# Kernel optimization log

Measured on AMD Instinct MI355X. Metric: run time of the kernel, lower is better.

## Reference

```python
import jax, jax.numpy as jnp
import numpy as np

N_HEAD = 32


def _apply_rope(x, rope):
    # x: (B, H, T, hs); rope: (block_size, hs//2) angles
    B, H, T, hs = x.shape
    ang = rope[:T]  # (T, hs//2)
    cos = jnp.cos(ang)[None, :, None, :]  # (1, T, 1, hs//2)
    sin = jnp.sin(ang)[None, :, None, :]
    xt = x.transpose(0, 2, 1, 3).reshape(B, T, H, hs // 2, 2)
    x0, x1 = xt[..., 0], xt[..., 1]
    out_r = x0 * cos - x1 * sin
    out_i = x0 * sin + x1 * cos
    out = jnp.stack([out_r, out_i], axis=-1).reshape(B, T, H, hs)
    return out.transpose(0, 2, 1, 3)


def setup_inputs() -> dict:
    key = jax.random.key(0)
    ks = jax.random.split(key, 6)
    B, T, C = 2, 2048, 4096
    aT = 10
    hs = C // N_HEAD
    return {
        "x": jax.random.normal(ks[0], (B, T, C), dtype=jnp.float32),
        "adaption_prompt": jax.random.normal(ks[1], (1, aT, C), dtype=jnp.float32),
        "rope_cache": jax.random.uniform(ks[2], (4096, hs // 2), dtype=jnp.float32) * 2.0 * np.pi,
        "w_attn": jax.random.normal(ks[3], (C, 3 * C), dtype=jnp.float32) * 0.02,
        "w_proj": jax.random.normal(ks[4], (C, C), dtype=jnp.float32) * 0.02,
        "gating_factor": jax.random.normal(ks[5], (1,), dtype=jnp.float32) * 0.1,
    }


def reference(x, adaption_prompt, rope_cache, w_attn, w_proj, gating_factor):
    B, T, C = x.shape
    H = N_HEAD
    hs = C // H

    qkv = x @ w_attn  # (B, T, 3C)
    q, k, v = jnp.split(qkv, 3, axis=2)
    q = q.reshape(B, T, H, hs).transpose(0, 2, 1, 3)  # (B, H, T, hs)
    k = k.reshape(B, T, H, hs).transpose(0, 2, 1, 3)
    v = v.reshape(B, T, H, hs).transpose(0, 2, 1, 3)

    q = _apply_rope(q, rope_cache)
    k = _apply_rope(k, rope_cache)

    # causal SDPA, scale = 1/sqrt(head_size)
    scale = 1.0 / jnp.sqrt(jnp.asarray(hs, dtype=q.dtype))
    scores = jnp.einsum("bhqd,bhkd->bhqk", q, k) * scale
    causal = jnp.tril(jnp.ones((T, T), dtype=bool))
    scores = jnp.where(causal[None, None, :, :], scores, jnp.asarray(-jnp.inf, scores.dtype))
    attn = jax.nn.softmax(scores, axis=-1)
    y = jnp.einsum("bhqk,bhkd->bhqd", attn, v)  # (B, H, T, hs)

    # adapter attention (note: scale uses full n_embd, as in source)
    aT = adaption_prompt.shape[1]
    aqkv = adaption_prompt @ w_attn  # (1, aT, 3C)
    _, ak, av = jnp.split(aqkv, 3, axis=2)
    ak = ak.reshape(1, aT, H, hs).transpose(0, 2, 1, 3)  # (1, H, aT, hs)
    av = av.reshape(1, aT, H, hs).transpose(0, 2, 1, 3)
    ascores = jnp.einsum("bhqd,xhkd->bhqk", q, ak) / jnp.sqrt(jnp.asarray(C, q.dtype))
    ascores = gating_factor[0] * jax.nn.softmax(ascores.astype(jnp.float32), axis=-1).astype(q.dtype)
    y = y + jnp.einsum("bhqk,xhkd->bhqd", ascores, av)

    y = y.transpose(0, 2, 1, 3).reshape(B, T, C)
    return y @ w_proj
```

## Files before the change

### kernel.cpp

```cpp
#include <hip/hip_runtime.h>

typedef unsigned short u16;
typedef unsigned int u32;
typedef __attribute__((ext_vector_type(4))) float f32x4;
typedef __attribute__((ext_vector_type(8))) _Float16 half8;
typedef __attribute__((ext_vector_type(8))) unsigned short u16x8;
typedef __attribute__((ext_vector_type(4))) unsigned short u16x4;

static __device__ __forceinline__ u16 f2h(float f) {
  union { _Float16 h; u16 u; } c;
  c.h = (_Float16)f;
  return c.u;
}
static __device__ __forceinline__ float h2f(u16 u) {
  union { _Float16 h; u16 u; } c;
  c.u = u;
  return (float)c.h;
}
static __device__ __forceinline__ void gload_lds16(const void* g, void* l) {
  __builtin_amdgcn_global_load_lds((const __attribute__((address_space(1))) void*)g,
                                   (__attribute__((address_space(3))) void*)l,
                                   16, 0, 0);
}

__global__ __launch_bounds__(256) void transpose_cvt(const float* __restrict__ src,
                                                     u16* __restrict__ dst,
                                                     int R, int C) {
  __shared__ float tt[64][65];
  const int t = threadIdx.x;
  const int c0 = blockIdx.x << 6, r0 = blockIdx.y << 6;
  const int r = t >> 4, cb = (t & 15) << 2;
#pragma unroll
  for (int i = 0; i < 4; ++i) {
    f32x4 v = *(const f32x4*)(src + (size_t)(r0 + r + i * 16) * C + c0 + cb);
#pragma unroll
    for (int j = 0; j < 4; ++j) tt[cb + j][r + i * 16] = v[j];
  }
  __syncthreads();
  const int cc = t >> 2, r8 = (t & 3) << 4;
  u16x8 o0, o1;
#pragma unroll
  for (int j = 0; j < 8; ++j) o0[j] = f2h(tt[cc][r8 + j]);
#pragma unroll
  for (int j = 0; j < 8; ++j) o1[j] = f2h(tt[cc][r8 + 8 + j]);
  u16* dp = dst + (size_t)(c0 + cc) * R + r0 + r8;
  *(u16x8*)dp = o0;
  *(u16x8*)(dp + 8) = o1;
}

__global__ __launch_bounds__(256) void cvt_f32_f16(const float* __restrict__ in,
                                                   u16* __restrict__ out, int n4) {
  int i = blockIdx.x * 256 + threadIdx.x;
  if (i >= n4) return;
  f32x4 v = *(const f32x4*)(in + (size_t)i * 4);
  u16x4 o;
  o[0] = f2h(v[0]); o[1] = f2h(v[1]); o[2] = f2h(v[2]); o[3] = f2h(v[3]);
  *(u16x4*)(out + (size_t)i * 4) = o;
}

static __device__ __forceinline__ void store_out(float* C, size_t idx, float v) { C[idx] = v; }
static __device__ __forceinline__ void store_out(u16* C, size_t idx, float v) { C[idx] = f2h(v); }

static __device__ __forceinline__ void stageA(const u16* __restrict__ Ab, int K, int kt,
                                              u16* As, int mh, int t) {
  int hf = t >> 8;
  int tt = t & 255;
  int row = hf * 128 + mh * 32 + (tt >> 3);
  int slot = tt & 7;
  gload_lds16(Ab + (size_t)row * K + kt + ((slot ^ (row & 7)) << 3),
              (char*)As + hf * 16384 + mh * 4096 + tt * 16);
}
static __device__ __forceinline__ void stageB(const u16* __restrict__ Bb, int K, int kt,
                                              u16* Bs, int j, int t) {
  int row = j * 64 + (t >> 3);
  int slot = t & 7;
  gload_lds16(Bb + (size_t)row * K + kt + ((slot ^ (row & 7)) << 3),
              (char*)Bs + j * 8192 + t * 16);
}

#define LOAD_BF(BS)                                                              \
  _Pragma("unroll") for (int nf = 0; nf < 4; ++nf)                               \
    _Pragma("unroll") for (int kk = 0; kk < 2; ++kk) {                           \
      int row = wn * 64 + nf * 16 + l15;                                         \
      int slot = (kk * 4 + g) ^ (l15 & 7);                                       \
      bf[nf][kk] = *(const half8*)((const char*)(BS) + row * 128 + slot * 16);   \
    }

#define LOAD_AF(AF, AS, Q)                                                       \
  _Pragma("unroll") for (int mf = 0; mf < 2; ++mf)                               \
    _Pragma("unroll") for (int kk = 0; kk < 2; ++kk) {                           \
      int row = wm * 128 + ((Q) * 2 + mf) * 16 + l15;                            \
      int slot = (kk * 4 + g) ^ (l15 & 7);                                       \
      (AF)[mf][kk] = *(const half8*)((const char*)(AS) + row * 128 + slot * 16); \
    }

#define MFMA_BURST(AF, Q)                                                        \
  __builtin_amdgcn_s_setprio(1);                                                 \
  _Pragma("unroll") for (int kk = 0; kk < 2; ++kk)                               \
    _Pragma("unroll") for (int mf = 0; mf < 2; ++mf)                             \
      _Pragma("unroll") for (int nf = 0; nf < 4; ++nf)                           \
        acc[(Q) * 2 + mf][nf] = __builtin_amdgcn_mfma_f32_16x16x32_f16(          \
            (AF)[mf][kk], bf[nf][kk], acc[(Q) * 2 + mf][nf], 0, 0, 0);           \
  __builtin_amdgcn_s_setprio(0);

template <typename OutT>
__global__ __launch_bounds__(512, 2) void gemm256(const u16* __restrict__ A,
                                                  const u16* __restrict__ Bt,
                                                  OutT* __restrict__ C,
                                                  u16* __restrict__ vtg,
                                                  int M, int N, int K, int nbn,
                                                  int ldc) {
  __shared__ u16 lds[4][16384];
  const int t = threadIdx.x;
  const int lane = t & 63;
  const int wid = t >> 6;
  const int g = lane >> 4, l15 = lane & 15;
  const int wm = wid >> 2, wn = wid & 3;
  const int nwg = gridDim.x;
  const int bid = blockIdx.x;
  const int wgid = (bid & 7) * (nwg >> 3) + (bid >> 3);
  const int bm = wgid / nbn, bn = wgid % nbn;
  const u16* Ab = A + (size_t)bm * 256 * K;
  const u16* Bb = Bt + (size_t)bn * 256 * K;
  f32x4 acc[8][4] = {};

  stageA(Ab, K, 0, lds[0], 0, t);
  stageA(Ab, K, 0, lds[0], 1, t);
  stageA(Ab, K, 0, lds[0], 2, t);
  stageA(Ab, K, 0, lds[0], 3, t);
  stageB(Bb, K, 0, lds[1], 0, t);
  stageB(Bb, K, 0, lds[1], 1, t);
  stageB(Bb, K, 0, lds[1], 2, t);
  stageB(Bb, K, 0, lds[1], 3, t);
  asm volatile("s_waitcnt vmcnt(0)" ::: "memory");
  __builtin_amdgcn_s_barrier();

  const int nt = K >> 6;
  for (int i = 0; i < nt; ++i) {
    u16* As  = lds[(i & 1) << 1];
    u16* Bs  = lds[((i & 1) << 1) + 1];
    u16* Asn = lds[((i + 1) & 1) << 1];
    u16* Bsn = lds[(((i + 1) & 1) << 1) + 1];
    int k1 = (i + 1) << 6; if (k1 >= K) k1 = 0;
    half8 bf[4][2], afA[2][2], afB[2][2];
    LOAD_BF(Bs);
    LOAD_AF(afA, As, 0);
    stageB(Bb, K, k1, Bsn, 0, t);
    stageB(Bb, K, k1, Bsn, 1, t);
    stageB(Bb, K, k1, Bsn, 2, t);
    stageB(Bb, K, k1, Bsn, 3, t);
    stageA(Ab, K, k1, Asn, 0, t);
    stageA(Ab, K, k1, Asn, 1, t);
    stageA(Ab, K, k1, Asn, 2, t);
    stageA(Ab, K, k1, Asn, 3, t);
    LOAD_AF(afB, As, 1);
    MFMA_BURST(afA, 0);
    LOAD_AF(afA, As, 2);
    MFMA_BURST(afB, 1);
    LOAD_AF(afB, As, 3);
    MFMA_BURST(afA, 2);
    MFMA_BURST(afB, 3);
    asm volatile("s_waitcnt vmcnt(0) lgkmcnt(0)" ::: "memory");
    __builtin_amdgcn_s_barrier();
  }

  if (vtg && bn >= 32) {
#pragma unroll
    for (int mf = 0; mf < 8; ++mf) {
      int row0 = bm * 256 + wm * 128 + mf * 16 + 4 * g;
      int bI = row0 >> 11, t0 = row0 & 2047;
#pragma unroll
      for (int nf = 0; nf < 4; ++nf) {
        int vcol = bn * 256 + wn * 64 + nf * 16 + l15 - 8192;
        int hI = vcol >> 7, dI = vcol & 127;
        u16x4 o;
#pragma unroll
        for (int r = 0; r < 4; ++r) o[r] = f2h(acc[mf][nf][r]);
        *(u16x4*)(vtg + ((size_t)(bI * 32 + hI) * 128 + dI) * 2048 + t0) = o;
      }
    }
  } else {
#pragma unroll
    for (int mf = 0; mf < 8; ++mf) {
      int row0 = bm * 256 + wm * 128 + mf * 16 + 4 * g;
#pragma unroll
      for (int nf = 0; nf < 4; ++nf) {
        int col = bn * 256 + wn * 64 + nf * 16 + l15;
#pragma unroll
        for (int r = 0; r < 4; ++r)
          store_out(C, (size_t)(row0 + r) * ldc + col, acc[mf][nf][r]);
      }
    }
  }
}

__global__ __launch_bounds__(256) void rope_kernel(u16* __restrict__ qk,
                                                   const float* __restrict__ rope) {
  int idx = blockIdx.x * 256 + threadIdx.x;
  int bt = idx >> 12;
  int pp = idx & 4095;
  int part = pp >> 11;
  int within = pp & 2047;
  int hh = within >> 6;
  int p = within & 63;
  int tpos = bt & 2047;
  size_t off = (size_t)bt * 8192 + part * 4096 + hh * 128 + 2 * p;
  u32* ptr = (u32*)(qk + off);
  u32 v = *ptr;
  float x0 = h2f((u16)(v & 0xffff));
  float x1 = h2f((u16)(v >> 16));
  float sn, cs;
  __sincosf(rope[tpos * 64 + p], &sn, &cs);
  float y0 = x0 * cs - x1 * sn;
  float y1 = x0 * sn + x1 * cs;
  *ptr = (u32)f2h(y0) | ((u32)f2h(y1) << 16);
}

__global__ __launch_bounds__(256) void adaption_kv_kernel(const float* __restrict__ prompt,
                                                          const float* __restrict__ w_attn,
                                                          u16* __restrict__ akbuf,
                                                          u16* __restrict__ avbuf) {
  __shared__ float pl[10][512];
  __shared__ float red[8][10][32];
  const int t = threadIdx.x;
  const int tc = t & 31, tk = t >> 5;
  const int n = blockIdx.x * 32 + tc;
  float acc[10] = {};
  for (int k0 = 0; k0 < 4096; k0 += 512) {
    __syncthreads();
#pragma unroll
    for (int i = 0; i < 20; ++i) {
      int idx = t + 256 * i;
      int j = idx >> 9, kk = idx & 511;
      pl[j][kk] = prompt[(size_t)j * 4096 + k0 + kk];
    }
    __syncthreads();
    for (int kk = tk; kk < 512; kk += 8) {
      float wv = w_attn[(size_t)(k0 + kk) * 12288 + 4096 + n];
#pragma unroll
      for (int j = 0; j < 10; ++j) acc[j] += pl[j][kk] * wv;
    }
  }
  __syncthreads();
#pragma unroll
  for (int j = 0; j < 10; ++j) red[tk][j][tc] = acc[j];
  __syncthreads();
  if (tk == 0) {
    float s[10];
#pragma unroll
    for (int j = 0; j < 10; ++j) {
      s[j] = 0.f;
#pragma unroll
      for (int q = 0; q < 8; ++q) s[j] += red[q][j][tc];
    }
    u16* dst;
    int hh, d;
    if (n < 4096) { dst = akbuf; hh = n >> 7; d = n & 127; }
    else          { dst = avbuf; hh = (n - 4096) >> 7; d = n & 127; }
#pragma unroll
    for (int j = 0; j < 16; ++j)
      dst[(size_t)(hh * 16 + j) * 128 + d] = (j < 10) ? f2h(s[j]) : (u16)0;
  }
}

__global__ __launch_bounds__(256) void attn_kernel(const u16* __restrict__ qk,
                                                   const u16* __restrict__ vt,
                                                   const u16* __restrict__ akbuf,
                                                   const u16* __restrict__ avbuf,
                                                   const float* __restrict__ gating,
                                                   u16* __restrict__ y) {
  __shared__ u16 Kl[64 * 128];
  __shared__ u16 Vtl[128 * 64];
  __shared__ u16 Pl[4][16 * 64];

  const int t = threadIdx.x;
  const int lane = t & 63, w = t >> 6;
  const int g = lane >> 4, l15 = lane & 15;
  const int bx = blockIdx.x;
  const int qb = 31 - (bx >> 6);
  const int bh = bx & 63, b = bh >> 5, h = bh & 31;
  const int ldq = 8192;
  const u16* Qg = qk + (size_t)b * 2048 * ldq + h * 128;
  const u16* Kg = Qg + 4096;
  const u16* VtG = vt + (size_t)(b * 32 + h) * 128 * 2048;
  u16* AKb = &Pl[0][0];

#pragma unroll
  for (int i = 0; i < 4; ++i) {
    int c = t + 256 * i;
    int row = c >> 4, slot = c & 15;
    gload_lds16(Qg + (size_t)(qb * 64 + row) * ldq + ((slot ^ (row & 15)) << 3),
                (char*)Kl + c * 16);
  }
  {
    int row = t >> 4, slot = t & 15;
    gload_lds16(akbuf + (size_t)(h * 16 + row) * 128 + ((slot ^ row) << 3),
                (char*)AKb + t * 16);
  }
  __syncthreads();

  half8 qf[4];
#pragma unroll
  for (int kk = 0; kk < 4; ++kk) {
    int slot = (kk * 4 + g) ^ l15;
    qf[kk] = *(const half8*)((const char*)Kl + (w * 16 + l15) * 256 + (slot << 4));
  }
  f32x4 sa = {};
#pragma unroll
  for (int kk = 0; kk < 4; ++kk) {
    int slot = (kk * 4 + g) ^ l15;
    half8 af = *(const half8*)((const char*)AKb + l15 * 256 + (slot << 4));
    sa = __builtin_amdgcn_mfma_f32_16x16x32_f16(qf[kk], af, sa, 0, 0, 0);
  }
  __syncthreads();

  f32x4 acc[8] = {};
  float mrun[4], lrun[4];
#pragma unroll
  for (int r = 0; r < 4; ++r) { mrun[r] = -1e30f; lrun[r] = 0.f; }

  for (int kvt = 0; kvt <= qb; ++kvt) {
#pragma unroll
    for (int i = 0; i < 4; ++i) {
      int c = t + 256 * i;
      int row = c >> 4, slot = c & 15;
      gload_lds16(Kg + (size_t)(kvt * 64 + row) * ldq + ((slot ^ (row & 15)) << 3),
                  (char*)Kl + c * 16);
    }
#pragma unroll
    for (int i = 0; i < 4; ++i) {
      int c = t + 256 * i;
      int d = c >> 3, s3 = c & 7;
      gload_lds16(VtG + (size_t)d * 2048 + kvt * 64 + ((s3 ^ (d & 7)) << 3),
                  (char*)Vtl + c * 16);
    }
    __syncthreads();

    f32x4 s[4] = {};
#pragma unroll
    for (int nf = 0; nf < 4; ++nf) {
#pragma unroll
      for (int kk = 0; kk < 4; ++kk) {
        int slot = (kk * 4 + g) ^ l15;
        half8 kf = *(const half8*)((const char*)Kl + (nf * 16 + l15) * 256 + (slot << 4));
        s[nf] = __builtin_amdgcn_mfma_f32_16x16x32_f16(qf[kk], kf, s[nf], 0, 0, 0);
      }
    }
    const float sc = 0.08838834764831843f;
    if (kvt == qb) {
#pragma unroll
      for (int nf = 0; nf < 4; ++nf)
#pragma unroll
        for (int r = 0; r < 4; ++r) {
          int kv = nf * 16 + l15;
          int qq = w * 16 + 4 * g + r;
          float v = s[nf][r] * sc;
          s[nf][r] = (kv <= qq) ? v : -1e30f;
        }
    } else {
#pragma unroll
      for (int nf = 0; nf < 4; ++nf)
#pragma unroll
        for (int r = 0; r < 4; ++r) s[nf][r] *= sc;
    }

    float alpha[4];
#pragma unroll
    for (int r = 0; r < 4; ++r) {
      float mt = fmaxf(fmaxf(s[0][r], s[1][r]), fmaxf(s[2][r], s[3][r]));
#pragma unroll
      for (int off = 1; off < 16; off <<= 1)
        mt = fmaxf(mt, __shfl_xor(mt, off, 64));
      float mn = fmaxf(mrun[r], mt);
      alpha[r] = __expf(mrun[r] - mn);
      mrun[r] = mn;
      float rs = 0.f;
#pragma unroll
      for (int nf = 0; nf < 4; ++nf) {
        float p = __expf(s[nf][r] - mn);
        s[nf][r] = p;
        rs += p;
      }
#pragma unroll
      for (int off = 1; off < 16; off <<= 1)
        rs += __shfl_xor(rs, off, 64);
      lrun[r] = lrun[r] * alpha[r] + rs;
    }
#pragma unroll
    for (int nd = 0; nd < 8; ++nd)
#pragma unroll
      for (int r = 0; r < 4; ++r)
        acc[nd][r] *= alpha[r];

#pragma unroll
    for (int nf = 0; nf < 4; ++nf)
#pragma unroll
      for (int r = 0; r < 4; ++r) {
        int qq = 4 * g + r;
        int kv = nf * 16 + l15;
        int byteoff = (qq * 128 + kv * 2) ^ ((qq & 7) << 4);
        *(u16*)((char*)Pl[w] + byteoff) = f2h(s[nf][r]);
      }

#pragma unroll
    for (int kk2 = 0; kk2 < 2; ++kk2) {
      int pslot = (kk2 * 4 + g) ^ (l15 & 7);
      half8 pf = *(const half8*)((const char*)Pl[w] + l15 * 128 + (pslot << 4));
#pragma unroll
      for (int nd = 0; nd < 8; ++nd) {
        int d = nd * 16 + l15;
        int slot = (kk2 * 4 + g) ^ (d & 7);
        half8 vf = *(const half8*)((const char*)Vtl + d * 128 + (slot << 4));
        acc[nd] = __builtin_amdgcn_mfma_f32_16x16x32_f16(pf, vf, acc[nd], 0, 0, 0);
      }
    }
    __syncthreads();
  }

  {
    int d = t >> 1;
    int jb = (t & 1) << 4;
#pragma unroll
    for (int i = 0; i < 16; ++i) {
      int j = jb + i;
      u16 v = (j < 16) ? avbuf[(size_t)(h * 16 + j) * 128 + d] : (u16)0;
      int byteoff = (d * 64 + j * 2) ^ ((d & 3) << 4);
      *(u16*)((char*)Kl + byteoff) = v;
    }
  }
  __syncthreads();

  float ga = gating[0];
  float pa4[4];
#pragma unroll
  for (int r = 0; r < 4; ++r) {
    float v = sa[r] * (1.0f / 64.0f);
    if (l15 >= 10) v = -1e30f;
    float mt = v;
#pragma unroll
    for (int off = 1; off < 16; off <<= 1)
      mt = fmaxf(mt, __shfl_xor(mt, off, 64));
    float p = __expf(v - mt);
    float rs = p;
#pragma unroll
    for (int off = 1; off < 16; off <<= 1)
      rs += __shfl_xor(rs, off, 64);
    pa4[r] = p / rs * ga;
  }
#pragma unroll
  for (int r = 0; r < 4; ++r) {
    float inv = 1.0f / lrun[r];
#pragma unroll
    for (int nd = 0; nd < 8; ++nd)
      acc[nd][r] *= inv;
  }
#pragma unroll
  for (int r = 0; r < 4; ++r) {
    int qq = 4 * g + r;
    int b1 = (qq * 128 + l15 * 2) ^ ((qq & 7) << 4);
    *(u16*)((char*)Pl[w] + b1) = f2h(pa4[r]);
    int b2 = (qq * 128 + (16 + l15) * 2) ^ ((qq & 7) << 4);
    *(u16*)((char*)Pl[w] + b2) = 0;
  }
  {
    int pslot = g ^ (l15 & 7);
    half8 pf = *(const half8*)((const char*)Pl[w] + l15 * 128 + (pslot << 4));
#pragma unroll
    for (int nd = 0; nd < 8; ++nd) {
      int d = nd * 16 + l15;
      int byteoff = (d * 64 + g * 16) ^ ((d & 3) << 4);
      half8 avf = *(const half8*)((const char*)Kl + byteoff);
      acc[nd] = __builtin_amdgcn_mfma_f32_16x16x32_f16(pf, avf, acc[nd], 0, 0, 0);
    }
  }
#pragma unroll
  for (int nd = 0; nd < 8; ++nd) {
    int col = h * 128 + nd * 16 + l15;
#pragma unroll
    for (int r = 0; r < 4; ++r) {
      int row = qb * 64 + w * 16 + 4 * g + r;
      y[(size_t)(b * 2048 + row) * 4096 + col] = f2h(acc[nd][r]);
    }
  }
}

extern "C" void kernel_launch(void* const* d_in, const int* in_sizes, int n_in,
                              void* d_out, int out_size, void* d_ws, size_t ws_size,
                              hipStream_t stream) {
  (void)in_sizes; (void)n_in; (void)out_size; (void)ws_size;
  const float* x      = (const float*)d_in[0];
  const float* prompt = (const float*)d_in[1];
  const float* rope   = (const float*)d_in[2];
  const float* w_attn = (const float*)d_in[3];
  const float* w_proj = (const float*)d_in[4];
  const float* gating = (const float*)d_in[5];
  float* out = (float*)d_out;

  char* ws = (char*)d_ws;
  u16* WtA = (u16*)(ws);
  u16* Yb  = (u16*)(ws);
  u16* qk  = (u16*)(ws + 100663296);
  u16* VtG = (u16*)(ws + 167772160);
  u16* xb  = (u16*)(ws + 201326592);
  u16* WtP = (u16*)(ws + 201326592);
  u16* akb = (u16*)(ws + 234881024);
  u16* avb = (u16*)(ws + 234881024 + 131072);

  transpose_cvt<<<dim3(192, 64), dim3(256), 0, stream>>>(w_attn, WtA, 4096, 12288);
  cvt_f32_f16<<<dim3(16384), dim3(256), 0, stream>>>(x, xb, 4194304);
  gemm256<u16><<<dim3(768), dim3(512), 0, stream>>>(xb, WtA, qk, VtG,
                                                    4096, 12288, 4096, 48, 8192);
  rope_kernel<<<dim3(65536), dim3(256), 0, stream>>>(qk, rope);
  adaption_kv_kernel<<<dim3(256), dim3(256), 0, stream>>>(prompt, w_attn, akb, avb);
  attn_kernel<<<dim3(2048), dim3(256), 0, stream>>>(qk, VtG, akb, avb, gating, Yb);
  transpose_cvt<<<dim3(64, 64), dim3(256), 0, stream>>>(w_proj, WtP, 4096, 4096);
  gemm256<float><<<dim3(256), dim3(512), 0, stream>>>(Yb, WtP, out, nullptr,
                                                      4096, 4096, 4096, 16, 4096);
}
```

Measured before the change: 985.5 us.

## Read Q/K/V fragments directly from global memory instead of staging through LDS

Removes the LDS staging of the Q tile, K tiles, V^T tiles and adapter K/V. Each wave now loads its MFMA operand fragments straight from global memory, which also drops the per-iteration __syncthreads barriers. This removes LDS traffic and synchronisation, but K and V tiles are now fetched by all four waves separately rather than shared through LDS. The kernel then depends on L1/L2 caching and on strided per-lane global loads, which may raise global memory traffic and latency.

```diff
diff --git a/kernel.cpp b/kernel.cpp
--- a/kernel.cpp
+++ b/kernel.cpp
@@ -269,8 +269,6 @@
                                                    const u16* __restrict__ avbuf,
                                                    const float* __restrict__ gating,
                                                    u16* __restrict__ y) {
-  __shared__ u16 Kl[64 * 128];
-  __shared__ u16 Vtl[128 * 64];
   __shared__ u16 Pl[4][16 * 64];
 
   const int t = threadIdx.x;
@@ -283,36 +281,23 @@
   const u16* Qg = qk + (size_t)b * 2048 * ldq + h * 128;
   const u16* Kg = Qg + 4096;
   const u16* VtG = vt + (size_t)(b * 32 + h) * 128 * 2048;
-  u16* AKb = &Pl[0][0];
-
-#pragma unroll
-  for (int i = 0; i < 4; ++i) {
-    int c = t + 256 * i;
-    int row = c >> 4, slot = c & 15;
-    gload_lds16(Qg + (size_t)(qb * 64 + row) * ldq + ((slot ^ (row & 15)) << 3),
-                (char*)Kl + c * 16);
-  }
+
+  half8 qf[4];
   {
-    int row = t >> 4, slot = t & 15;
-    gload_lds16(akbuf + (size_t)(h * 16 + row) * 128 + ((slot ^ row) << 3),
-                (char*)AKb + t * 16);
-  }
-  __syncthreads();
-
-  half8 qf[4];
-#pragma unroll
-  for (int kk = 0; kk < 4; ++kk) {
-    int slot = (kk * 4 + g) ^ l15;
-    qf[kk] = *(const half8*)((const char*)Kl + (w * 16 + l15) * 256 + (slot << 4));
+    const u16* qrow = Qg + (size_t)(qb * 64 + w * 16 + l15) * ldq;
+#pragma unroll
+    for (int kk = 0; kk < 4; ++kk)
+      qf[kk] = *(const half8*)(qrow + kk * 32 + g * 8);
   }
   f32x4 sa = {};
-#pragma unroll
-  for (int kk = 0; kk < 4; ++kk) {
-    int slot = (kk * 4 + g) ^ l15;
-    half8 af = *(const half8*)((const char*)AKb + l15 * 256 + (slot << 4));
-    sa = __builtin_amdgcn_mfma_f32_16x16x32_f16(qf[kk], af, sa, 0, 0, 0);
-  }
-  __syncthreads();
+  {
+    const u16* arow = akbuf + (size_t)(h * 16 + l15) * 128;
+#pragma unroll
+    for (int kk = 0; kk < 4; ++kk) {
+      half8 af = *(const half8*)(arow + kk * 32 + g * 8);
+      sa = __builtin_amdgcn_mfma_f32_16x16x32_f16(qf[kk], af, sa, 0, 0, 0);
+    }
+  }
 
   f32x4 acc[8] = {};
   float mrun[4], lrun[4];
@@ -320,29 +305,13 @@
   for (int r = 0; r < 4; ++r) { mrun[r] = -1e30f; lrun[r] = 0.f; }
 
   for (int kvt = 0; kvt <= qb; ++kvt) {
-#pragma unroll
-    for (int i = 0; i < 4; ++i) {
-      int c = t + 256 * i;
-      int row = c >> 4, slot = c & 15;
-      gload_lds16(Kg + (size_t)(kvt * 64 + row) * ldq + ((slot ^ (row & 15)) << 3),
-                  (char*)Kl + c * 16);
-    }
-#pragma unroll
-    for (int i = 0; i < 4; ++i) {
-      int c = t + 256 * i;
-      int d = c >> 3, s3 = c & 7;
-      gload_lds16(VtG + (size_t)d * 2048 + kvt * 64 + ((s3 ^ (d & 7)) << 3),
-                  (char*)Vtl + c * 16);
-    }
-    __syncthreads();
-
     f32x4 s[4] = {};
 #pragma unroll
     for (int nf = 0; nf < 4; ++nf) {
+      const u16* krow = Kg + (size_t)(kvt * 64 + nf * 16 + l15) * ldq;
 #pragma unroll
       for (int kk = 0; kk < 4; ++kk) {
-        int slot = (kk * 4 + g) ^ l15;
-        half8 kf = *(const half8*)((const char*)Kl + (nf * 16 + l15) * 256 + (slot << 4));
+        half8 kf = *(const half8*)(krow + kk * 32 + g * 8);
         s[nf] = __builtin_amdgcn_mfma_f32_16x16x32_f16(qf[kk], kf, s[nf], 0, 0, 0);
       }
     }
@@ -409,26 +378,11 @@
 #pragma unroll
       for (int nd = 0; nd < 8; ++nd) {
         int d = nd * 16 + l15;
-        int slot = (kk2 * 4 + g) ^ (d & 7);
-        half8 vf = *(const half8*)((const char*)Vtl + d * 128 + (slot << 4));
+        half8 vf = *(const half8*)(VtG + (size_t)d * 2048 + kvt * 64 + kk2 * 32 + g * 8);
         acc[nd] = __builtin_amdgcn_mfma_f32_16x16x32_f16(pf, vf, acc[nd], 0, 0, 0);
       }
     }
-    __syncthreads();
-  }
-
-  {
-    int d = t >> 1;
-    int jb = (t & 1) << 4;
-#pragma unroll
-    for (int i = 0; i < 16; ++i) {
-      int j = jb + i;
-      u16 v = (j < 16) ? avbuf[(size_t)(h * 16 + j) * 128 + d] : (u16)0;
-      int byteoff = (d * 64 + j * 2) ^ ((d & 3) << 4);
-      *(u16*)((char*)Kl + byteoff) = v;
-    }
-  }
-  __syncthreads();
+  }
 
   float ga = gating[0];
   float pa4[4];
@@ -468,8 +422,16 @@
 #pragma unroll
     for (int nd = 0; nd < 8; ++nd) {
       int d = nd * 16 + l15;
-      int byteoff = (d * 64 + g * 16) ^ ((d & 3) << 4);
-      half8 avf = *(const half8*)((const char*)Kl + byteoff);
+      half8 avf = {};
+      if (g < 2) {
+        const u16* avp = avbuf + (size_t)(h * 16 + g * 8) * 128 + d;
+#pragma unroll
+        for (int jj = 0; jj < 8; ++jj) {
+          union { _Float16 h; u16 u; } c;
+          c.u = avp[(size_t)jj * 128];
+          avf[jj] = c.h;
+        }
+      }
       acc[nd] = __builtin_amdgcn_mfma_f32_16x16x32_f16(pf, avf, acc[nd], 0, 0, 0);
     }
   }
```

After: 1.332 ms. 35.2% more time.
